# Kernel optimization log

Measured on AMD Instinct MI355X. Metric: run time of the kernel, lower is better.

Reference implementation:

```python
import jax, jax.numpy as jnp
import numpy as np

B, S, D, FF, E = 4, 2048, 1024, 4096, 8


def setup_inputs() -> dict:
    key = jax.random.key(0)
    ks = jax.random.split(key, 6)
    scale_r = 1.0 / np.sqrt(D)
    return {
        "x": jax.random.normal(ks[0], (B, S, D), dtype=jnp.float32),
        "W_router": jax.random.normal(ks[1], (D, E), dtype=jnp.float32) * scale_r,
        "W1": jax.random.normal(ks[2], (E, D, FF), dtype=jnp.float32) * (1.0 / np.sqrt(D)),
        "b1": jnp.zeros((E, FF), dtype=jnp.float32),
        "W2": jax.random.normal(ks[3], (E, FF, D), dtype=jnp.float32) * (1.0 / np.sqrt(FF)),
        "b2": jnp.zeros((E, D), dtype=jnp.float32),
    }


def reference(x, W_router, W1, b1, W2, b2):
    # Router: softmax over experts, top-2, renormalize the 2 gates with softmax
    logits = jnp.einsum("bsd,de->bse", x, W_router)          # [B,S,E]
    probs = jax.nn.softmax(logits, axis=-1)
    top_vals, top_idx = jax.lax.top_k(probs, 2)               # [B,S,2]
    gates2 = jax.nn.softmax(top_vals, axis=-1)                # [B,S,2]

    num_experts = W1.shape[0]
    out = jnp.zeros_like(x)
    # Faithful masked-dense MoE: each expert runs over all tokens (input masked),
    # output scaled by its gate (0 for non-selected tokens).
    for i in range(num_experts):
        sel = (top_idx == i)                                  # [B,S,2] bool
        mask = jnp.any(sel, axis=-1, keepdims=True).astype(x.dtype)  # [B,S,1]
        xi = x * mask
        h = jax.nn.gelu(jnp.einsum("bsd,df->bsf", xi, W1[i]) + b1[i], approximate=False)
        yi = jnp.einsum("bsf,fd->bsd", h, W2[i]) + b2[i]
        g = jnp.sum(gates2 * sel.astype(x.dtype), axis=-1, keepdims=True)  # [B,S,1]
        out = out + yi * g
    return out
```

## Files before the change

### kernel.cpp

```cpp
#include <hip/hip_runtime.h>
#include <hip/hip_bf16.h>
#include <math.h>

#define NEXP 8
#define DDIM 1024
#define FFDIM 4096
#define NTOK 8192
#define NSLOT (NTOK * 2)
#define BM 128
#define BN 128
#define BK 64
#define MAXT ((NSLOT / BM) + NEXP)

typedef __attribute__((ext_vector_type(8))) __bf16 bf16x8;
typedef __attribute__((ext_vector_type(4))) float f32x4;

union BF8 { __bf16 b[8]; uint4 u; bf16x8 v; };

__device__ __forceinline__ float gelu_exact(float v) {
    return 0.5f * v * (1.0f + erff(v * 0.70710678118654752f));
}

__device__ __forceinline__ int swz(int row, int colb) {
    return row * 128 + (colb ^ ((row & 7) << 4));
}

typedef const __attribute__((address_space(1))) void* gptr1_t;
typedef __attribute__((address_space(3))) void* lptr3_t;
__device__ __forceinline__ void gll16(const void* g, void* l) {
    __builtin_amdgcn_global_load_lds((gptr1_t)g, (lptr3_t)l, 16, 0, 0);
}

__global__ __launch_bounds__(64)
void router_kernel(const float* __restrict__ x, const float* __restrict__ Wr,
                   int* __restrict__ idx2, float* __restrict__ gates2,
                   int* __restrict__ counts)
{
    int t = blockIdx.x;
    int lane = threadIdx.x;
    const float* xr = x + (size_t)t * DDIM;
    float acc[NEXP];
#pragma unroll
    for (int e = 0; e < NEXP; ++e) acc[e] = 0.f;
    for (int d = lane; d < DDIM; d += 64) {
        float xv = xr[d];
        const float* wrow = Wr + d * NEXP;
#pragma unroll
        for (int e = 0; e < NEXP; ++e) acc[e] += xv * wrow[e];
    }
#pragma unroll
    for (int e = 0; e < NEXP; ++e) {
        float v = acc[e];
        for (int off = 32; off > 0; off >>= 1) v += __shfl_xor(v, off, 64);
        acc[e] = v;
    }
    if (lane == 0) {
        float mx = acc[0];
#pragma unroll
        for (int e = 1; e < NEXP; ++e) mx = fmaxf(mx, acc[e]);
        float p[NEXP]; float s = 0.f;
#pragma unroll
        for (int e = 0; e < NEXP; ++e) { p[e] = expf(acc[e] - mx); s += p[e]; }
        float inv = 1.f / s;
#pragma unroll
        for (int e = 0; e < NEXP; ++e) p[e] *= inv;
        int i1 = 0; float p1 = p[0];
#pragma unroll
        for (int e = 1; e < NEXP; ++e) if (p[e] > p1) { p1 = p[e]; i1 = e; }
        int i2 = -1; float p2 = -1.f;
#pragma unroll
        for (int e = 0; e < NEXP; ++e) {
            if (e == i1) continue;
            if (p[e] > p2) { p2 = p[e]; i2 = e; }
        }
        float u = expf(p2 - p1);
        float den = 1.f + u;
        idx2[2 * t] = i1; idx2[2 * t + 1] = i2;
        gates2[2 * t] = 1.f / den; gates2[2 * t + 1] = u / den;
        atomicAdd(&counts[i1], 1);
        atomicAdd(&counts[i2], 1);
    }
}

__global__ __launch_bounds__(256)
void offsets_kernel(const int* __restrict__ counts, int* __restrict__ offsets,
                    int* __restrict__ cursors, int* __restrict__ tiletab)
{
    __shared__ int soff[NEXP], stile[NEXP + 1];
    int tid = threadIdx.x;
    if (tid == 0) {
        int off = 0, tt = 0;
        for (int e = 0; e < NEXP; ++e) {
            soff[e] = off; stile[e] = tt;
            int c = counts[e];
            off += c; tt += (c + BM - 1) / BM;
        }
        stile[NEXP] = tt;
    }
    __syncthreads();
    if (tid < NEXP) { offsets[tid] = soff[tid]; cursors[tid] = 0; }
    int total = stile[NEXP];
    for (int i = tid; i < MAXT; i += 256) {
        if (i < total) {
            int e = 0;
            while (stile[e + 1] <= i) ++e;
            tiletab[2 * i] = e; tiletab[2 * i + 1] = i - stile[e];
        } else {
            tiletab[2 * i] = -1; tiletab[2 * i + 1] = 0;
        }
    }
}

__global__ __launch_bounds__(256)
void fill_kernel(const int* __restrict__ idx2, const float* __restrict__ gates2,
                 const int* __restrict__ offsets, int* __restrict__ cursors,
                 int* __restrict__ perm, float* __restrict__ gate_slot,
                 int* __restrict__ tslot)
{
    int t = blockIdx.x * 256 + threadIdx.x;
    if (t >= NTOK) return;
#pragma unroll
    for (int s = 0; s < 2; ++s) {
        int e = idx2[2 * t + s];
        int pos = atomicAdd(&cursors[e], 1);
        int slot = offsets[e] + pos;
        perm[slot] = t;
        gate_slot[slot] = gates2[2 * t + s];
        tslot[2 * t + s] = slot;
    }
}

__global__ __launch_bounds__(256)
void convert_x_kernel(const float* __restrict__ x, __bf16* __restrict__ xb)
{
    size_t i = ((size_t)blockIdx.x * 256 + threadIdx.x) * 8;
    float4 a = *(const float4*)(x + i);
    float4 b = *(const float4*)(x + i + 4);
    BF8 pk;
    pk.b[0] = (__bf16)a.x; pk.b[1] = (__bf16)a.y; pk.b[2] = (__bf16)a.z; pk.b[3] = (__bf16)a.w;
    pk.b[4] = (__bf16)b.x; pk.b[5] = (__bf16)b.y; pk.b[6] = (__bf16)b.z; pk.b[7] = (__bf16)b.w;
    *(uint4*)(xb + i) = pk.u;
}

__global__ __launch_bounds__(128)
void convert_w_kernel(const float* __restrict__ W, __bf16* __restrict__ WT, int K, int N)
{
    int ktiles = K >> 6;
    int nt = blockIdx.x / ktiles;
    int kt = blockIdx.x % ktiles;
    int e = blockIdx.y;
    const float* We = W + (size_t)e * K * N;
    int r = threadIdx.x;
    const float* src = We + (size_t)(kt * 64) * N + nt * 128 + r;
    char* dst = (char*)WT + ((((size_t)e * (N >> 7) + nt) * ktiles + kt) << 14) + r * 128;
    float f[64];
#pragma unroll
    for (int j = 0; j < 64; ++j) f[j] = src[(size_t)j * N];
#pragma unroll
    for (int gi = 0; gi < 8; ++gi) {
        BF8 pk;
#pragma unroll
        for (int q = 0; q < 8; ++q) pk.b[q] = (__bf16)f[gi * 8 + q];
        *(uint4*)(dst + ((gi * 16) ^ ((r & 7) << 4))) = pk.u;
    }
}

__device__ __forceinline__ bool tile_header(const int* counts, const int* offsets,
                                            const int* tiletab, int e_arg, int c_arg, int CH,
                                            int& e, int& start, int& cnt, int& hbase, int& row0,
                                            int& rows_here)
{
    int rowtile;
    if (e_arg >= 0) {
        e = e_arg;
        int cbase = c_arg * CH;
        cnt = counts[e] - cbase;
        if (cnt <= 0) return false;
        if (cnt > CH) cnt = CH;
        start = offsets[e] + cbase;
        rowtile = blockIdx.y;
        hbase = start;
    } else {
        e = tiletab[2 * blockIdx.y];
        if (e < 0) return false;
        rowtile = tiletab[2 * blockIdx.y + 1];
        start = offsets[e];
        cnt = counts[e];
        hbase = 0;
    }
    row0 = rowtile * BM;
    if (row0 >= cnt) return false;
    rows_here = cnt - row0;
    if (rows_here > BM) rows_here = BM;
    return true;
}

__global__ __launch_bounds__(256)
void gemm1_fast(const __bf16* __restrict__ xb, const __bf16* __restrict__ W1T,
                const float* __restrict__ b1,
                const int* __restrict__ perm, const int* __restrict__ counts,
                const int* __restrict__ offsets, const int* __restrict__ tiletab,
                __bf16* __restrict__ H, int e_arg, int c_arg, int CH)
{
    __shared__ __align__(16) char smem[(BM + BN) * 128];
    char* As = smem;
    char* Bs = smem + BM * 128;

    int e, start, cnt, hbase, row0, rows_here;
    if (!tile_header(counts, offsets, tiletab, e_arg, c_arg, CH, e, start, cnt, hbase, row0, rows_here))
        return;

    const float* b1e = b1 + (size_t)e * FFDIM;
    int nt = blockIdx.x;
    int n0 = nt * BN;
    const char* bsrc = (const char*)W1T + ((((size_t)e * (FFDIM >> 7) + nt) * (DDIM >> 6)) << 14);

    int tid = threadIdx.x;
    int lane = tid & 63;
    int wid = tid >> 6;
    int wm = wid >> 1, wn = wid & 1;
    int lr = lane & 15, lhi = lane >> 4;

    int laneswz = (((lane & 7) ^ (lane >> 3)) << 4);
    const char* xrowp[4];
#pragma unroll
    for (int j = 0; j < 4; ++j) {
        int rr = wid * 32 + j * 8 + (lane >> 3);
        int re = rr < rows_here ? rr : 0;
        int tok = perm[start + row0 + re];
        xrowp[j] = (const char*)(xb + (size_t)tok * DDIM);
    }
    char* aldsb = As + wid * 4096;
    char* bldsb = Bs + wid * 4096;
    const char* bwave = bsrc + wid * 4096 + lane * 16;

    f32x4 acc[4][4] = {};

    for (int kt = 0; kt < DDIM / BK; ++kt) {
        __syncthreads();
#pragma unroll
        for (int j = 0; j < 4; ++j)
            gll16(xrowp[j] + kt * 128 + laneswz, aldsb + j * 1024);
#pragma unroll
        for (int j = 0; j < 4; ++j)
            gll16(bwave + ((size_t)kt << 14) + j * 1024, bldsb + j * 1024);
        __syncthreads();

#pragma unroll
        for (int kk = 0; kk < 2; ++kk) {
            bf16x8 af[4], bfr[4];
#pragma unroll
            for (int m = 0; m < 4; ++m)
                af[m] = *(const bf16x8*)(As + swz(wm * 64 + m * 16 + lr, kk * 64 + lhi * 16));
#pragma unroll
            for (int n = 0; n < 4; ++n)
                bfr[n] = *(const bf16x8*)(Bs + swz(wn * 64 + n * 16 + lr, kk * 64 + lhi * 16));
#pragma unroll
            for (int m = 0; m < 4; ++m)
#pragma unroll
                for (int n = 0; n < 4; ++n)
                    acc[m][n] = __builtin_amdgcn_mfma_f32_16x16x32_bf16(af[m], bfr[n], acc[m][n], 0, 0, 0);
        }
    }

    float bias[4];
#pragma unroll
    for (int n = 0; n < 4; ++n) bias[n] = b1e[n0 + wn * 64 + n * 16 + lr];

#pragma unroll
    for (int m = 0; m < 4; ++m) {
        int rbase = wm * 64 + m * 16 + lhi * 4;
#pragma unroll
        for (int j = 0; j < 4; ++j) {
            int rl = rbase + j;
            if (rl < rows_here) {
                __bf16* hr = H + (size_t)(start + row0 + rl - hbase) * FFDIM + n0 + wn * 64;
#pragma unroll
                for (int n = 0; n < 4; ++n) {
                    float v = acc[m][n][j] + bias[n];
                    hr[n * 16 + lr] = (__bf16)gelu_exact(v);
                }
            }
        }
    }
}

__global__ __launch_bounds__(256)
void gemm2_fast(const __bf16* __restrict__ H, const __bf16* __restrict__ W2T,
                const float* __restrict__ b2,
                const int* __restrict__ perm, const float* __restrict__ gate_slot,
                const int* __restrict__ counts, const int* __restrict__ offsets,
                const int* __restrict__ tiletab,
                float* __restrict__ out, float* __restrict__ Y, int use_y,
                int e_arg, int c_arg, int CH)
{
    __shared__ __align__(16) char smem[(BM + BN) * 128];
    char* As = smem;
    char* Bs = smem + BM * 128;

    int e, start, cnt, hbase, row0, rows_here;
    if (!tile_header(counts, offsets, tiletab, e_arg, c_arg, CH, e, start, cnt, hbase, row0, rows_here))
        return;

    const float* b2e = b2 + (size_t)e * DDIM;
    int nt = blockIdx.x;
    int n0 = nt * BN;
    const char* bsrc = (const char*)W2T + ((((size_t)e * (DDIM >> 7) + nt) * (FFDIM >> 6)) << 14);

    int tid = threadIdx.x;
    int lane = tid & 63;
    int wid = tid >> 6;
    int wm = wid >> 1, wn = wid & 1;
    int lr = lane & 15, lhi = lane >> 4;

    int laneswz = (((lane & 7) ^ (lane >> 3)) << 4);
    const char* hrowp[4];
#pragma unroll
    for (int j = 0; j < 4; ++j) {
        int rr = wid * 32 + j * 8 + (lane >> 3);
        int re = rr < rows_here ? rr : 0;
        hrowp[j] = (const char*)(H + (size_t)(start + row0 + re - hbase) * FFDIM);
    }
    char* aldsb = As + wid * 4096;
    char* bldsb = Bs + wid * 4096;
    const char* bwave = bsrc + wid * 4096 + lane * 16;

    f32x4 acc[4][4] = {};

    for (int kt = 0; kt < FFDIM / BK; ++kt) {
        __syncthreads();
#pragma unroll
        for (int j = 0; j < 4; ++j)
            gll16(hrowp[j] + kt * 128 + laneswz, aldsb + j * 1024);
#pragma unroll
        for (int j = 0; j < 4; ++j)
            gll16(bwave + ((size_t)kt << 14) + j * 1024, bldsb + j * 1024);
        __syncthreads();

#pragma unroll
        for (int kk = 0; kk < 2; ++kk) {
            bf16x8 af[4], bfr[4];
#pragma unroll
            for (int m = 0; m < 4; ++m)
                af[m] = *(const bf16x8*)(As + swz(wm * 64 + m * 16 + lr, kk * 64 + lhi * 16));
#pragma unroll
            for (int n = 0; n < 4; ++n)
                bfr[n] = *(const bf16x8*)(Bs + swz(wn * 64 + n * 16 + lr, kk * 64 + lhi * 16));
#pragma unroll
            for (int m = 0; m < 4; ++m)
#pragma unroll
                for (int n = 0; n < 4; ++n)
                    acc[m][n] = __builtin_amdgcn_mfma_f32_16x16x32_bf16(af[m], bfr[n], acc[m][n], 0, 0, 0);
        }
    }

    float bias[4];
#pragma unroll
    for (int n = 0; n < 4; ++n) bias[n] = b2e[n0 + wn * 64 + n * 16 + lr];

#pragma unroll
    for (int m = 0; m < 4; ++m) {
        int rbase = wm * 64 + m * 16 + lhi * 4;
#pragma unroll
        for (int j = 0; j < 4; ++j) {
            int rl = rbase + j;
            if (rl < rows_here) {
                int slot = start + row0 + rl;
                float g = gate_slot[slot];
                if (use_y) {
                    float* yrow = Y + (size_t)slot * DDIM + n0 + wn * 64;
#pragma unroll
                    for (int n = 0; n < 4; ++n)
                        yrow[n * 16 + lr] = (acc[m][n][j] + bias[n]) * g;
                } else {
                    int token = perm[slot];
                    float* orow = out + (size_t)token * DDIM + n0 + wn * 64;
#pragma unroll
                    for (int n = 0; n < 4; ++n)
                        atomicAdd(orow + n * 16 + lr, (acc[m][n][j] + bias[n]) * g);
                }
            }
        }
    }
}

__global__ __launch_bounds__(256)
void combine_kernel(const float* __restrict__ Y, const int* __restrict__ tslot,
                    float* __restrict__ out)
{
    int t = blockIdx.x;
    int c = threadIdx.x * 4;
    int sa = tslot[2 * t], sb = tslot[2 * t + 1];
    float4 a = *(const float4*)(Y + (size_t)sa * DDIM + c);
    float4 b = *(const float4*)(Y + (size_t)sb * DDIM + c);
    float4 r;
    r.x = a.x + b.x; r.y = a.y + b.y; r.z = a.z + b.z; r.w = a.w + b.w;
    *(float4*)(out + (size_t)t * DDIM + c) = r;
}

__global__ __launch_bounds__(256)
void gemm1_legacy(const float* __restrict__ x, const float* __restrict__ W1,
                  const float* __restrict__ b1,
                  const int* __restrict__ perm, const int* __restrict__ counts,
                  const int* __restrict__ offsets, const int* __restrict__ tiletab,
                  __bf16* __restrict__ H, int e_arg, int c_arg, int CH)
{
    __shared__ __align__(16) char smem[(BM + BN) * 128];
    char* As = smem;
    char* Bs = smem + BM * 128;

    int e, start, cnt, hbase, row0, rows_here;
    if (!tile_header(counts, offsets, tiletab, e_arg, c_arg, CH, e, start, cnt, hbase, row0, rows_here))
        return;

    const float* W1e = W1 + (size_t)e * DDIM * FFDIM;
    const float* b1e = b1 + (size_t)e * FFDIM;
    int n0 = blockIdx.x * BN;

    int tid = threadIdx.x;
    int lane = tid & 63;
    int wid = tid >> 6;
    int wm = wid >> 1, wn = wid & 1;
    int lr = lane & 15, lhi = lane >> 4;

    int ar = tid >> 1, ach = tid & 1;
    int token = -1;
    if (ar < rows_here) token = perm[start + row0 + ar];
    const float* arow = x + (size_t)(token < 0 ? 0 : token) * DDIM + ach * 32;

    int bn = tid & 127, bkh = tid >> 7;
    const float* bcol = W1e + (size_t)bkh * 32 * FFDIM + n0 + bn;

    f32x4 acc[4][4] = {};

    for (int k0 = 0; k0 < DDIM; k0 += BK) {
        __syncthreads();
        {
            BF8 pk[4];
            if (token >= 0) {
                const float4* p = (const float4*)(arow + k0);
#pragma unroll
                for (int i = 0; i < 4; ++i) {
                    float4 v0 = p[2 * i], v1 = p[2 * i + 1];
                    pk[i].b[0] = (__bf16)v0.x; pk[i].b[1] = (__bf16)v0.y;
                    pk[i].b[2] = (__bf16)v0.z; pk[i].b[3] = (__bf16)v0.w;
                    pk[i].b[4] = (__bf16)v1.x; pk[i].b[5] = (__bf16)v1.y;
                    pk[i].b[6] = (__bf16)v1.z; pk[i].b[7] = (__bf16)v1.w;
                }
            } else {
#pragma unroll
                for (int i = 0; i < 4; ++i) pk[i].u = make_uint4(0u, 0u, 0u, 0u);
            }
#pragma unroll
            for (int i = 0; i < 4; ++i)
                *(uint4*)(As + swz(ar, ach * 64 + i * 16)) = pk[i].u;
        }
        {
            float f[32];
            const float* p = bcol + (size_t)k0 * FFDIM;
#pragma unroll
            for (int j = 0; j < 32; ++j) f[j] = p[(size_t)j * FFDIM];
#pragma unroll
            for (int i = 0; i < 4; ++i) {
                BF8 pk;
#pragma unroll
                for (int q = 0; q < 8; ++q) pk.b[q] = (__bf16)f[i * 8 + q];
                *(uint4*)(Bs + swz(bn, bkh * 64 + i * 16)) = pk.u;
            }
        }
        __syncthreads();

#pragma unroll
        for (int kk = 0; kk < 2; ++kk) {
            bf16x8 af[4], bfr[4];
#pragma unroll
            for (int m = 0; m < 4; ++m)
                af[m] = *(const bf16x8*)(As + swz(wm * 64 + m * 16 + lr, kk * 64 + lhi * 16));
#pragma unroll
            for (int n = 0; n < 4; ++n)
                bfr[n] = *(const bf16x8*)(Bs + swz(wn * 64 + n * 16 + lr, kk * 64 + lhi * 16));
#pragma unroll
            for (int m = 0; m < 4; ++m)
#pragma unroll
                for (int n = 0; n < 4; ++n)
                    acc[m][n] = __builtin_amdgcn_mfma_f32_16x16x32_bf16(af[m], bfr[n], acc[m][n], 0, 0, 0);
        }
    }

    float bias[4];
#pragma unroll
    for (int n = 0; n < 4; ++n) bias[n] = b1e[n0 + wn * 64 + n * 16 + lr];

#pragma unroll
    for (int m = 0; m < 4; ++m) {
        int rbase = wm * 64 + m * 16 + lhi * 4;
#pragma unroll
        for (int j = 0; j < 4; ++j) {
            int rl = rbase + j;
            if (rl < rows_here) {
                __bf16* hr = H + (size_t)(start + row0 + rl - hbase) * FFDIM + n0 + wn * 64;
#pragma unroll
                for (int n = 0; n < 4; ++n) {
                    float v = acc[m][n][j] + bias[n];
                    hr[n * 16 + lr] = (__bf16)gelu_exact(v);
                }
            }
        }
    }
}

__global__ __launch_bounds__(256)
void gemm2_legacy(const __bf16* __restrict__ H, const float* __restrict__ W2,
                  const float* __restrict__ b2,
                  const int* __restrict__ perm, const float* __restrict__ gate_slot,
                  const int* __restrict__ counts, const int* __restrict__ offsets,
                  const int* __restrict__ tiletab,
                  float* __restrict__ out, int e_arg, int c_arg, int CH)
{
    __shared__ __align__(16) char smem[(BM + BN) * 128];
    char* As = smem;
    char* Bs = smem + BM * 128;

    int e, start, cnt, hbase, row0, rows_here;
    if (!tile_header(counts, offsets, tiletab, e_arg, c_arg, CH, e, start, cnt, hbase, row0, rows_here))
        return;

    const float* W2e = W2 + (size_t)e * FFDIM * DDIM;
    const float* b2e = b2 + (size_t)e * DDIM;
    int n0 = blockIdx.x * BN;

    int tid = threadIdx.x;
    int lane = tid & 63;
    int wid = tid >> 6;
    int wm = wid >> 1, wn = wid & 1;
    int lr = lane & 15, lhi = lane >> 4;

    int ar = tid >> 1, ach = tid & 1;
    bool aval = (ar < rows_here);
    const __bf16* hrow = H + (size_t)(aval ? (start + row0 + ar - hbase) : 0) * FFDIM + ach * 32;

    int bn = tid & 127, bkh = tid >> 7;
    const float* bcol = W2e + (size_t)bkh * 32 * DDIM + n0 + bn;

    f32x4 acc[4][4] = {};

    for (int k0 = 0; k0 < FFDIM; k0 += BK) {
        __syncthreads();
        {
            uint4 v[4];
            if (aval) {
                const uint4* p = (const uint4*)(hrow + k0);
#pragma unroll
                for (int i = 0; i < 4; ++i) v[i] = p[i];
            } else {
#pragma unroll
                for (int i = 0; i < 4; ++i) v[i] = make_uint4(0u, 0u, 0u, 0u);
            }
#pragma unroll
            for (int i = 0; i < 4; ++i)
                *(uint4*)(As + swz(ar, ach * 64 + i * 16)) = v[i];
        }
        {
            float f[32];
            const float* p = bcol + (size_t)k0 * DDIM;
#pragma unroll
            for (int j = 0; j < 32; ++j) f[j] = p[(size_t)j * DDIM];
#pragma unroll
            for (int i = 0; i < 4; ++i) {
                BF8 pk;
#pragma unroll
                for (int q = 0; q < 8; ++q) pk.b[q] = (__bf16)f[i * 8 + q];
                *(uint4*)(Bs + swz(bn, bkh * 64 + i * 16)) = pk.u;
            }
        }
        __syncthreads();

#pragma unroll
        for (int kk = 0; kk < 2; ++kk) {
            bf16x8 af[4], bfr[4];
#pragma unroll
            for (int m = 0; m < 4; ++m)
                af[m] = *(const bf16x8*)(As + swz(wm * 64 + m * 16 + lr, kk * 64 + lhi * 16));
#pragma unroll
            for (int n = 0; n < 4; ++n)
                bfr[n] = *(const bf16x8*)(Bs + swz(wn * 64 + n * 16 + lr, kk * 64 + lhi * 16));
#pragma unroll
            for (int m = 0; m < 4; ++m)
#pragma unroll
                for (int n = 0; n < 4; ++n)
                    acc[m][n] = __builtin_amdgcn_mfma_f32_16x16x32_bf16(af[m], bfr[n], acc[m][n], 0, 0, 0);
        }
    }

    float bias[4];
#pragma unroll
    for (int n = 0; n < 4; ++n) bias[n] = b2e[n0 + wn * 64 + n * 16 + lr];

#pragma unroll
    for (int m = 0; m < 4; ++m) {
        int rbase = wm * 64 + m * 16 + lhi * 4;
#pragma unroll
        for (int j = 0; j < 4; ++j) {
            int rl = rbase + j;
            if (rl < rows_here) {
                int slot = start + row0 + rl;
                int token = perm[slot];
                float g = gate_slot[slot];
                float* orow = out + (size_t)token * DDIM + n0 + wn * 64;
#pragma unroll
                for (int n = 0; n < 4; ++n) {
                    float v = (acc[m][n][j] + bias[n]) * g;
                    atomicAdd(orow + n * 16 + lr, v);
                }
            }
        }
    }
}

extern "C" void kernel_launch(void* const* d_in, const int* in_sizes, int n_in,
                              void* d_out, int out_size, void* d_ws, size_t ws_size,
                              hipStream_t stream)
{
    const float* x  = (const float*)d_in[0];
    const float* Wr = (const float*)d_in[1];
    const float* W1 = (const float*)d_in[2];
    const float* b1 = (const float*)d_in[3];
    const float* W2 = (const float*)d_in[4];
    const float* b2 = (const float*)d_in[5];
    float* out = (float*)d_out;

    char* ws = (char*)d_ws;
    int* counts   = (int*)ws;
    int* offsets  = counts + 8;
    int* cursors  = offsets + 8;
    int* tiletab  = cursors + 8;
    int* idx2     = tiletab + 2 * MAXT;
    float* gates2 = (float*)(idx2 + 2 * NTOK);
    int* perm     = (int*)(gates2 + 2 * NTOK);
    float* gate_slot = (float*)(perm + NSLOT);
    int* tslot    = (int*)(gate_slot + NSLOT);
    char* hraw = (char*)(tslot + 2 * NTOK);
    size_t small_end = (((size_t)(hraw - ws)) + 255) & ~(size_t)255;

    __bf16* xb  = (__bf16*)(ws + small_end);
    __bf16* W1T = xb + (size_t)NTOK * DDIM;
    __bf16* W2T = W1T + (size_t)NEXP * DDIM * FFDIM;
    __bf16* Hf  = W2T + (size_t)NEXP * FFDIM * DDIM;
    float*  Y   = (float*)W1T;
    size_t fast_off = small_end + ((size_t)NTOK * DDIM + 2 * (size_t)NEXP * DDIM * FFDIM) * 2;
    size_t availHf = ws_size > fast_off ? ws_size - fast_off : 0;
    size_t need_H = (size_t)NSLOT * FFDIM * 2;
    bool have_w = availHf >= (size_t)BM * FFDIM * 2 * 8;

    hipMemsetAsync(counts, 0, 8 * sizeof(int), stream);

    router_kernel<<<NTOK, 64, 0, stream>>>(x, Wr, idx2, gates2, counts);
    if (have_w) {
        convert_x_kernel<<<NTOK * DDIM / 2048, 256, 0, stream>>>(x, xb);
        convert_w_kernel<<<dim3((FFDIM / 128) * (DDIM / 64), NEXP), 128, 0, stream>>>(W1, W1T, DDIM, FFDIM);
        convert_w_kernel<<<dim3((DDIM / 128) * (FFDIM / 64), NEXP), 128, 0, stream>>>(W2, W2T, FFDIM, DDIM);
    }
    offsets_kernel<<<1, 256, 0, stream>>>(counts, offsets, cursors, tiletab);
    fill_kernel<<<NTOK / 256, 256, 0, stream>>>(idx2, gates2, offsets, cursors, perm, gate_slot, tslot);

    if (have_w && availHf >= need_H) {
        dim3 g1(FFDIM / BN, MAXT, 1);
        gemm1_fast<<<g1, 256, 0, stream>>>(xb, W1T, b1, perm, counts, offsets, tiletab, Hf, -1, 0, 0);
        dim3 g2(DDIM / BN, MAXT, 1);
        gemm2_fast<<<g2, 256, 0, stream>>>(Hf, W2T, b2, perm, gate_slot, counts, offsets, tiletab,
                                           out, Y, 1, -1, 0, 0);
        combine_kernel<<<NTOK, 256, 0, stream>>>(Y, tslot, out);
    } else if (have_w) {
        hipMemsetAsync(d_out, 0, (size_t)out_size * sizeof(float), stream);
        long long chl = (long long)((availHf / ((size_t)FFDIM * 2)) / BM) * BM;
        int CH = (int)(chl > 4096 ? 4096 : chl);
        int nchunk = (NSLOT + CH - 1) / CH;
        for (int e = 0; e < NEXP; ++e) {
            for (int c = 0; c < nchunk; ++c) {
                dim3 g1(FFDIM / BN, CH / BM, 1);
                gemm1_fast<<<g1, 256, 0, stream>>>(xb, W1T, b1, perm, counts, offsets, tiletab, Hf, e, c, CH);
                dim3 g2(DDIM / BN, CH / BM, 1);
                gemm2_fast<<<g2, 256, 0, stream>>>(Hf, W2T, b2, perm, gate_slot, counts, offsets, tiletab,
                                                   out, (float*)nullptr, 0, e, c, CH);
            }
        }
    } else {
        hipMemsetAsync(d_out, 0, (size_t)out_size * sizeof(float), stream);
        __bf16* H = (__bf16*)(ws + small_end);
        size_t avail = ws_size > small_end ? ws_size - small_end : 0;
        if (avail >= need_H) {
            dim3 g1(FFDIM / BN, MAXT, 1);
            gemm1_legacy<<<g1, 256, 0, stream>>>(x, W1, b1, perm, counts, offsets, tiletab, H, -1, 0, 0);
            dim3 g2(DDIM / BN, MAXT, 1);
            gemm2_legacy<<<g2, 256, 0, stream>>>(H, W2, b2, perm, gate_slot, counts, offsets, tiletab, out, -1, 0, 0);
        } else {
            long long chl = (long long)((avail / ((size_t)FFDIM * 2)) / BM) * BM;
            int CH = (int)(chl > 2048 ? 2048 : chl);
            if (CH >= BM) {
                int nchunk = (NSLOT + CH - 1) / CH;
                for (int e = 0; e < NEXP; ++e) {
                    for (int c = 0; c < nchunk; ++c) {
                        dim3 g1(FFDIM / BN, CH / BM, 1);
                        gemm1_legacy<<<g1, 256, 0, stream>>>(x, W1, b1, perm, counts, offsets, tiletab, H, e, c, CH);
                        dim3 g2(DDIM / BN, CH / BM, 1);
                        gemm2_legacy<<<g2, 256, 0, stream>>>(H, W2, b2, perm, gate_slot, counts, offsets, tiletab, out, e, c, CH);
                    }
                }
            }
        }
    }
}
```

Baseline: 956.4 us.

## Register-prefetch GEMM tiles, remap blocks across XCDs, raise occupancy hint

Both expert GEMM kernels drop the direct global-to-LDS loads and instead prefetch the next K-tile into registers while the current tile is being multiplied, then store it to swizzled LDS. The 2D grid is flattened to 1D, and block IDs are remapped so that consecutive row tiles sharing a weight column tile land on the same XCD, which is meant to improve L2 reuse of the weights. Launch bounds now request 4 blocks per CU. The costs are more registers and extra LDS store instructions, since the direct-to-LDS path is gone.

```diff
diff --git a/kernel.cpp b/kernel.cpp
--- a/kernel.cpp
+++ b/kernel.cpp
@@ -25,10 +25,9 @@
     return row * 128 + (colb ^ ((row & 7) << 4));
 }
 
-typedef const __attribute__((address_space(1))) void* gptr1_t;
-typedef __attribute__((address_space(3))) void* lptr3_t;
-__device__ __forceinline__ void gll16(const void* g, void* l) {
-    __builtin_amdgcn_global_load_lds((gptr1_t)g, (lptr3_t)l, 16, 0, 0);
+__device__ __forceinline__ int xcd_logical(int bid, int nwg) {
+    if (nwg & 7) return bid;
+    return (bid & 7) * (nwg >> 3) + (bid >> 3);
 }
 
 __global__ __launch_bounds__(64)
@@ -167,6 +166,7 @@
 
 __device__ __forceinline__ bool tile_header(const int* counts, const int* offsets,
                                             const int* tiletab, int e_arg, int c_arg, int CH,
+                                            int tile_idx,
                                             int& e, int& start, int& cnt, int& hbase, int& row0,
                                             int& rows_here)
 {
@@ -178,12 +178,12 @@
         if (cnt <= 0) return false;
         if (cnt > CH) cnt = CH;
         start = offsets[e] + cbase;
-        rowtile = blockIdx.y;
+        rowtile = tile_idx;
         hbase = start;
     } else {
-        e = tiletab[2 * blockIdx.y];
+        e = tiletab[2 * tile_idx];
         if (e < 0) return false;
-        rowtile = tiletab[2 * blockIdx.y + 1];
+        rowtile = tiletab[2 * tile_idx + 1];
         start = offsets[e];
         cnt = counts[e];
         hbase = 0;
@@ -195,7 +195,7 @@
     return true;
 }
 
-__global__ __launch_bounds__(256)
+__global__ __launch_bounds__(256, 4)
 void gemm1_fast(const __bf16* __restrict__ xb, const __bf16* __restrict__ W1T,
                 const float* __restrict__ b1,
                 const int* __restrict__ perm, const int* __restrict__ counts,
@@ -206,12 +206,20 @@
     char* As = smem;
     char* Bs = smem + BM * 128;
 
+    int tile_idx, nt;
+    if (e_arg >= 0) { nt = blockIdx.x; tile_idx = blockIdx.y; }
+    else {
+        int L = xcd_logical(blockIdx.x, gridDim.x);
+        tile_idx = L % MAXT;
+        nt = L / MAXT;
+    }
+
     int e, start, cnt, hbase, row0, rows_here;
-    if (!tile_header(counts, offsets, tiletab, e_arg, c_arg, CH, e, start, cnt, hbase, row0, rows_here))
+    if (!tile_header(counts, offsets, tiletab, e_arg, c_arg, CH, tile_idx,
+                     e, start, cnt, hbase, row0, rows_here))
         return;
 
     const float* b1e = b1 + (size_t)e * FFDIM;
-    int nt = blockIdx.x;
     int n0 = nt * BN;
     const char* bsrc = (const char*)W1T + ((((size_t)e * (FFDIM >> 7) + nt) * (DDIM >> 6)) << 14);
 
@@ -221,30 +229,43 @@
     int wm = wid >> 1, wn = wid & 1;
     int lr = lane & 15, lhi = lane >> 4;
 
-    int laneswz = (((lane & 7) ^ (lane >> 3)) << 4);
-    const char* xrowp[4];
-#pragma unroll
-    for (int j = 0; j < 4; ++j) {
-        int rr = wid * 32 + j * 8 + (lane >> 3);
-        int re = rr < rows_here ? rr : 0;
-        int tok = perm[start + row0 + re];
-        xrowp[j] = (const char*)(xb + (size_t)tok * DDIM);
-    }
-    char* aldsb = As + wid * 4096;
-    char* bldsb = Bs + wid * 4096;
-    const char* bwave = bsrc + wid * 4096 + lane * 16;
+    int ar = tid >> 1, ach = tid & 1;
+    int token = -1;
+    if (ar < rows_here) token = perm[start + row0 + ar];
+    const __bf16* arow = xb + (size_t)(token < 0 ? 0 : token) * DDIM + ach * 32;
+    int boff = wid * 4096 + lane * 16;
+
+    uint4 av[4], bv[4];
+#define G1_LOAD_A(kt)                                                     \
+    if (token >= 0) {                                                     \
+        const uint4* p = (const uint4*)(arow + (kt) * BK);                \
+        av[0] = p[0]; av[1] = p[1]; av[2] = p[2]; av[3] = p[3];           \
+    } else {                                                              \
+        av[0] = av[1] = av[2] = av[3] = make_uint4(0u, 0u, 0u, 0u);       \
+    }
+#define G1_LOAD_B(kt) {                                                   \
+        const char* tsrc = bsrc + ((size_t)(kt) << 14);                   \
+        bv[0] = *(const uint4*)(tsrc + 0 * 1024 + boff);                  \
+        bv[1] = *(const uint4*)(tsrc + 1 * 1024 + boff);                  \
+        bv[2] = *(const uint4*)(tsrc + 2 * 1024 + boff);                  \
+        bv[3] = *(const uint4*)(tsrc + 3 * 1024 + boff);                  \
+    }
+
+    G1_LOAD_A(0); G1_LOAD_B(0);
 
     f32x4 acc[4][4] = {};
 
     for (int kt = 0; kt < DDIM / BK; ++kt) {
         __syncthreads();
 #pragma unroll
+        for (int i = 0; i < 4; ++i)
+            *(uint4*)(As + swz(ar, ach * 64 + i * 16)) = av[i];
+#pragma unroll
         for (int j = 0; j < 4; ++j)
-            gll16(xrowp[j] + kt * 128 + laneswz, aldsb + j * 1024);
-#pragma unroll
-        for (int j = 0; j < 4; ++j)
-            gll16(bwave + ((size_t)kt << 14) + j * 1024, bldsb + j * 1024);
+            *(uint4*)(Bs + j * 1024 + boff) = bv[j];
         __syncthreads();
+
+        if (kt + 1 < DDIM / BK) { G1_LOAD_A(kt + 1); G1_LOAD_B(kt + 1); }
 
 #pragma unroll
         for (int kk = 0; kk < 2; ++kk) {
@@ -285,7 +306,7 @@
     }
 }
 
-__global__ __launch_bounds__(256)
+__global__ __launch_bounds__(256, 4)
 void gemm2_fast(const __bf16* __restrict__ H, const __bf16* __restrict__ W2T,
                 const float* __restrict__ b2,
                 const int* __restrict__ perm, const float* __restrict__ gate_slot,
@@ -298,12 +319,20 @@
     char* As = smem;
     char* Bs = smem + BM * 128;
 
+    int tile_idx, nt;
+    if (e_arg >= 0) { nt = blockIdx.x; tile_idx = blockIdx.y; }
+    else {
+        int L = xcd_logical(blockIdx.x, gridDim.x);
+        tile_idx = L % MAXT;
+        nt = L / MAXT;
+    }
+
     int e, start, cnt, hbase, row0, rows_here;
-    if (!tile_header(counts, offsets, tiletab, e_arg, c_arg, CH, e, start, cnt, hbase, row0, rows_here))
+    if (!tile_header(counts, offsets, tiletab, e_arg, c_arg, CH, tile_idx,
+                     e, start, cnt, hbase, row0, rows_here))
         return;
 
     const float* b2e = b2 + (size_t)e * DDIM;
-    int nt = blockIdx.x;
     int n0 = nt * BN;
     const char* bsrc = (const char*)W2T + ((((size_t)e * (DDIM >> 7) + nt) * (FFDIM >> 6)) << 14);
 
@@ -313,29 +342,42 @@
     int wm = wid >> 1, wn = wid & 1;
     int lr = lane & 15, lhi = lane >> 4;
 
-    int laneswz = (((lane & 7) ^ (lane >> 3)) << 4);
-    const char* hrowp[4];
-#pragma unroll
-    for (int j = 0; j < 4; ++j) {
-        int rr = wid * 32 + j * 8 + (lane >> 3);
-        int re = rr < rows_here ? rr : 0;
-        hrowp[j] = (const char*)(H + (size_t)(start + row0 + re - hbase) * FFDIM);
-    }
-    char* aldsb = As + wid * 4096;
-    char* bldsb = Bs + wid * 4096;
-    const char* bwave = bsrc + wid * 4096 + lane * 16;
+    int ar = tid >> 1, ach = tid & 1;
+    bool aval = (ar < rows_here);
+    const __bf16* hrow = H + (size_t)(aval ? (start + row0 + ar - hbase) : 0) * FFDIM + ach * 32;
+    int boff = wid * 4096 + lane * 16;
+
+    uint4 av[4], bv[4];
+#define G2_LOAD_A(kt)                                                     \
+    if (aval) {                                                           \
+        const uint4* p = (const uint4*)(hrow + (kt) * BK);                \
+        av[0] = p[0]; av[1] = p[1]; av[2] = p[2]; av[3] = p[3];           \
+    } else {                                                              \
+        av[0] = av[1] = av[2] = av[3] = make_uint4(0u, 0u, 0u, 0u);       \
+    }
+#define G2_LOAD_B(kt) {                                                   \
+        const char* tsrc = bsrc + ((size_t)(kt) << 14);                   \
+        bv[0] = *(const uint4*)(tsrc + 0 * 1024 + boff);                  \
+        bv[1] = *(const uint4*)(tsrc + 1 * 1024 + boff);                  \
+        bv[2] = *(const uint4*)(tsrc + 2 * 1024 + boff);                  \
+        bv[3] = *(const uint4*)(tsrc + 3 * 1024 + boff);                  \
+    }
+
+    G2_LOAD_A(0); G2_LOAD_B(0);
 
     f32x4 acc[4][4] = {};
 
     for (int kt = 0; kt < FFDIM / BK; ++kt) {
         __syncthreads();
 #pragma unroll
+        for (int i = 0; i < 4; ++i)
+            *(uint4*)(As + swz(ar, ach * 64 + i * 16)) = av[i];
+#pragma unroll
         for (int j = 0; j < 4; ++j)
-            gll16(hrowp[j] + kt * 128 + laneswz, aldsb + j * 1024);
-#pragma unroll
-        for (int j = 0; j < 4; ++j)
-            gll16(bwave + ((size_t)kt << 14) + j * 1024, bldsb + j * 1024);
+            *(uint4*)(Bs + j * 1024 + boff) = bv[j];
         __syncthreads();
+
+        if (kt + 1 < FFDIM / BK) { G2_LOAD_A(kt + 1); G2_LOAD_B(kt + 1); }
 
 #pragma unroll
         for (int kk = 0; kk < 2; ++kk) {
@@ -410,7 +452,8 @@
     char* Bs = smem + BM * 128;
 
     int e, start, cnt, hbase, row0, rows_here;
-    if (!tile_header(counts, offsets, tiletab, e_arg, c_arg, CH, e, start, cnt, hbase, row0, rows_here))
+    if (!tile_header(counts, offsets, tiletab, e_arg, c_arg, CH, blockIdx.y,
+                     e, start, cnt, hbase, row0, rows_here))
         return;
 
     const float* W1e = W1 + (size_t)e * DDIM * FFDIM;
@@ -522,7 +565,8 @@
     char* Bs = smem + BM * 128;
 
     int e, start, cnt, hbase, row0, rows_here;
-    if (!tile_header(counts, offsets, tiletab, e_arg, c_arg, CH, e, start, cnt, hbase, row0, rows_here))
+    if (!tile_header(counts, offsets, tiletab, e_arg, c_arg, CH, blockIdx.y,
+                     e, start, cnt, hbase, row0, rows_here))
         return;
 
     const float* W2e = W2 + (size_t)e * FFDIM * DDIM;
@@ -664,11 +708,10 @@
     fill_kernel<<<NTOK / 256, 256, 0, stream>>>(idx2, gates2, offsets, cursors, perm, gate_slot, tslot);
 
     if (have_w && availHf >= need_H) {
-        dim3 g1(FFDIM / BN, MAXT, 1);
-        gemm1_fast<<<g1, 256, 0, stream>>>(xb, W1T, b1, perm, counts, offsets, tiletab, Hf, -1, 0, 0);
-        dim3 g2(DDIM / BN, MAXT, 1);
-        gemm2_fast<<<g2, 256, 0, stream>>>(Hf, W2T, b2, perm, gate_slot, counts, offsets, tiletab,
-                                           out, Y, 1, -1, 0, 0);
+        gemm1_fast<<<(FFDIM / BN) * MAXT, 256, 0, stream>>>(xb, W1T, b1, perm, counts, offsets,
+                                                            tiletab, Hf, -1, 0, 0);
+        gemm2_fast<<<(DDIM / BN) * MAXT, 256, 0, stream>>>(Hf, W2T, b2, perm, gate_slot, counts,
+                                                           offsets, tiletab, out, Y, 1, -1, 0, 0);
         combine_kernel<<<NTOK, 256, 0, stream>>>(Y, tslot, out);
     } else if (have_w) {
         hipMemsetAsync(d_out, 0, (size_t)out_size * sizeof(float), stream);
```

Result: slower. 1.395 ms (+45.9%).
